# Optimization experiments

Measured on AMD Instinct MI355X. Metric: run time of the kernel, lower is better.

Reference implementation:

```python
import jax, jax.numpy as jnp
import numpy as np

HEADS = 2
C1 = 33    # per-head out channels, conv1
C2 = 550   # per-head out channels, conv2


def _lin_params(key, fan_in, fan_out):
    kw, kb = jax.random.split(key)
    scale = 1.0 / np.sqrt(fan_in)
    W = jax.random.uniform(kw, (fan_in, fan_out), jnp.float32, -scale, scale)
    b = jax.random.uniform(kb, (fan_out,), jnp.float32, -scale, scale)
    return W, b


def transformer_conv(x, src, dst, Wq, bq, Wk, bk, Wv, bv, Ws, bs, heads, out_ch):
    """PyG TransformerConv (concat=True, root_weight=True, beta=False)."""
    N = x.shape[0]
    q = (x @ Wq + bq).reshape(N, heads, out_ch)  # query of target node i
    k = (x @ Wk + bk).reshape(N, heads, out_ch)  # key of source node j
    v = (x @ Wv + bv).reshape(N, heads, out_ch)  # value of source node j
    # attention logits per edge: [E, H]
    alpha = jnp.einsum('ehc,ehc->eh', q[dst], k[src]) / jnp.sqrt(jnp.float32(out_ch))
    # segment softmax over incoming edges of each dst node
    m = jax.lax.stop_gradient(jax.ops.segment_max(alpha, dst, num_segments=N))  # [N,H]
    e = jnp.exp(alpha - m[dst])
    denom = jax.ops.segment_sum(e, dst, num_segments=N)  # [N,H]
    a = e / denom[dst]
    # weighted scatter-aggregate of source values: [N,H,C]
    out = jax.ops.segment_sum(a[..., None] * v[src], dst, num_segments=N)
    out = out.reshape(N, heads * out_ch)
    # root/skip connection
    out = out + x @ Ws + bs
    return out


def setup_inputs() -> dict:
    key = jax.random.key(0)
    ks = jax.random.split(key, 10)
    N, E, IN = 20000, 120000, 256
    x = jax.random.normal(ks[0], (N, IN), jnp.float32)
    edge_index = jax.random.randint(ks[1], (2, E), 0, N, jnp.int64 if jax.config.jax_enable_x64 else jnp.int32)
    d = {'x': x, 'edge_index': edge_index}
    # conv1: IN -> heads*C1
    d['Wq1'], d['bq1'] = _lin_params(ks[2], IN, HEADS * C1)
    d['Wk1'], d['bk1'] = _lin_params(ks[3], IN, HEADS * C1)
    d['Wv1'], d['bv1'] = _lin_params(ks[4], IN, HEADS * C1)
    d['Ws1'], d['bs1'] = _lin_params(ks[5], IN, HEADS * C1)
    # conv2: heads*C1 -> heads*C2
    IN2 = HEADS * C1
    d['Wq2'], d['bq2'] = _lin_params(ks[6], IN2, HEADS * C2)
    d['Wk2'], d['bk2'] = _lin_params(ks[7], IN2, HEADS * C2)
    d['Wv2'], d['bv2'] = _lin_params(ks[8], IN2, HEADS * C2)
    d['Ws2'], d['bs2'] = _lin_params(ks[9], IN2, HEADS * C2)
    return d


def reference(x, edge_index, Wq1, bq1, Wk1, bk1, Wv1, bv1, Ws1, bs1,
              Wq2, bq2, Wk2, bk2, Wv2, bv2, Ws2, bs2):
    src, dst = edge_index[0], edge_index[1]
    h = transformer_conv(x, src, dst, Wq1, bq1, Wk1, bk1, Wv1, bv1, Ws1, bs1, HEADS, C1)
    h = transformer_conv(h, src, dst, Wq2, bq2, Wk2, bk2, Wv2, bv2, Ws2, bs2, HEADS, C2)
    # x.view(N, 550, heads).max(dim=2) -- faithful to the original reshape layout
    h = h.reshape(h.shape[0], C2, HEADS)
    return jnp.max(h, axis=2)
```

## Files before the change

kernel.cpp:

```cpp
#include <hip/hip_runtime.h>
#include <math.h>

#define HEADS 2
#define C1    33
#define C2    550
#define D1    66
#define D2    1100
#define IN1   256
#define PROJW 288
#define KU    224
#define N2P   1152
#define KZ    96
#define ZW    144

typedef __attribute__((ext_vector_type(8))) short bfrag;
typedef __attribute__((ext_vector_type(4))) float f32x4;

__device__ inline unsigned short f2bf(float f) {
    unsigned int u = __float_as_uint(f);
    u += 0x7FFFu + ((u >> 16) & 1u);
    return (unsigned short)(u >> 16);
}

__device__ inline int xcd_slot(int bid, int slots) {
    return (bid >> 3) + (bid & 7) * slots;
}

__global__ void k_cvt(const float* __restrict__ x, unsigned short* __restrict__ xb, int total4) {
    int i = blockIdx.x * blockDim.x + threadIdx.x;
    if (i >= total4) return;
    float4 v = ((const float4*)x)[i];
    ushort4 o;
    o.x = f2bf(v.x); o.y = f2bf(v.y); o.z = f2bf(v.z); o.w = f2bf(v.w);
    ((ushort4*)xb)[i] = o;
}

__global__ void k_prep1(const float* __restrict__ Wq, const float* __restrict__ bq,
                        const float* __restrict__ Wk, const float* __restrict__ bk,
                        const float* __restrict__ Wv, const float* __restrict__ bv,
                        const float* __restrict__ Ws, const float* __restrict__ bs,
                        unsigned short* __restrict__ Wt1, float* __restrict__ bcat) {
    int c = blockIdx.x;
    int k = threadIdx.x;
    float val = 0.f, bia = 0.f;
    if (c < 4 * D1) {
        int m = c / D1, j = c % D1;
        const float* W; const float* B;
        switch (m) {
            case 0: W = Wq; B = bq; break;
            case 1: W = Wk; B = bk; break;
            case 2: W = Wv; B = bv; break;
            default: W = Ws; B = bs; break;
        }
        val = W[(size_t)k * D1 + j];
        bia = B[j];
    }
    Wt1[(size_t)c * IN1 + k] = f2bf(val);
    if (k == 0) bcat[c] = bia;
}

__global__ void k_prep2(const float* __restrict__ Wv2, const float* __restrict__ bv2,
                        const float* __restrict__ Ws2, const float* __restrict__ bs2,
                        unsigned short* __restrict__ W2t,
                        float* __restrict__ bvp, float* __restrict__ bsp) {
    int c = blockIdx.x;
    int k = threadIdx.x;
    if (k < KU) {
        float val = 0.f;
        if (c < D2) {
            int h = (c >= C2) ? 1 : 0;
            if (!h) {
                if (k < 66) val = Wv2[(size_t)k * D2 + c];
                else if (k >= 132 && k < 198) val = Ws2[(size_t)(k - 132) * D2 + c];
            } else {
                if (k >= 66 && k < 132) val = Wv2[(size_t)(k - 66) * D2 + c];
                else if (k >= 132 && k < 198) val = Ws2[(size_t)(k - 132) * D2 + c];
            }
        }
        W2t[(size_t)c * KU + k] = f2bf(val);
    }
    if (k == 0) {
        bvp[c] = (c < D2) ? bv2[c] : 0.f;
        bsp[c] = (c < D2) ? bs2[c] : 0.f;
    }
}

__global__ void k_hist(const int* __restrict__ dst, int E, int* __restrict__ cnt) {
    int e = blockIdx.x * blockDim.x + threadIdx.x;
    if (e < E) atomicAdd(&cnt[dst[e]], 1);
}

__global__ void k_scan(const int* __restrict__ cnt, int* __restrict__ roff,
                       int* __restrict__ pos, int N) {
    __shared__ int wsum[16];
    __shared__ int carry_s;
    int tid = threadIdx.x, wid = tid >> 6, lane = tid & 63;
    if (tid == 0) { carry_s = 0; roff[0] = 0; }
    __syncthreads();
    for (int base = 0; base < N; base += 1024) {
        int i = base + tid;
        int v = (i < N) ? cnt[i] : 0;
        int x = v;
        #pragma unroll
        for (int s = 1; s < 64; s <<= 1) {
            int t = __shfl_up(x, s, 64);
            if (lane >= s) x += t;
        }
        if (lane == 63) wsum[wid] = x;
        __syncthreads();
        if (tid < 16) {
            int y = wsum[tid];
            #pragma unroll
            for (int s = 1; s < 16; s <<= 1) {
                int t = __shfl_up(y, s, 16);
                if (tid >= s) y += t;
            }
            wsum[tid] = y;
        }
        __syncthreads();
        int carry = carry_s;
        int incl = carry + (wid ? wsum[wid - 1] : 0) + x;
        if (i < N) { roff[i + 1] = incl; pos[i] = incl - v; }
        __syncthreads();
        if (tid == 0) carry_s = carry + wsum[15];
        __syncthreads();
    }
}

__global__ void k_fill(const int* __restrict__ src, const int* __restrict__ dst, int E,
                       int* __restrict__ pos, int* __restrict__ elist) {
    int e = blockIdx.x * blockDim.x + threadIdx.x;
    if (e < E) {
        int slot = atomicAdd(&pos[dst[e]], 1);
        elist[slot] = src[e];
    }
}

__global__ __launch_bounds__(256, 2) void k_mm1(
        const unsigned short* __restrict__ A, const unsigned short* __restrict__ B,
        const float* __restrict__ bias, float* __restrict__ proj, int N,
        int nRow, int slots) {
    __shared__ __align__(16) short bs[8 * 4 * 96 * 8];
    int s = xcd_slot(blockIdx.x, slots);
    if (s >= nRow * 3) return;
    int rowt = s / 3, g = s - rowt * 3;
    int cbase = g * 96;
    int tid = threadIdx.x;
    for (int i = tid; i < 3072; i += 256) {
        int ks = i / 384, r = i % 384;
        int lk = r / 96, col = r % 96;
        *(bfrag*)&bs[i * 8] = *(const bfrag*)(B + (size_t)(cbase + col) * IN1 + ks * 32 + lk * 8);
    }
    int wave = tid >> 6, lane = tid & 63;
    int lr = lane & 15, lk = lane >> 4;
    int rbase = rowt * 128 + wave * 32;
    int ar[2];
    #pragma unroll
    for (int mi = 0; mi < 2; mi++) {
        int r = rbase + mi * 16 + lr;
        ar[mi] = (r < N) ? r : (N - 1);
    }
    bfrag a[2][8];
    #pragma unroll
    for (int mi = 0; mi < 2; mi++)
        #pragma unroll
        for (int ks = 0; ks < 8; ks++)
            a[mi][ks] = *(const bfrag*)(A + (size_t)ar[mi] * IN1 + ks * 32 + lk * 8);
    __syncthreads();
    f32x4 acc[2][6];
    #pragma unroll
    for (int mi = 0; mi < 2; mi++)
        #pragma unroll
        for (int ni = 0; ni < 6; ni++) acc[mi][ni] = (f32x4){0.f, 0.f, 0.f, 0.f};
    #pragma unroll
    for (int ks = 0; ks < 8; ks++) {
        bfrag b[6];
        #pragma unroll
        for (int ni = 0; ni < 6; ni++)
            b[ni] = *(const bfrag*)&bs[ks * 3072 + lk * 768 + (ni * 16 + lr) * 8];
        #pragma unroll
        for (int mi = 0; mi < 2; mi++)
            #pragma unroll
            for (int ni = 0; ni < 6; ni++)
                acc[mi][ni] = __builtin_amdgcn_mfma_f32_16x16x32_bf16(a[mi][ks], b[ni], acc[mi][ni], 0, 0, 0);
    }
    #pragma unroll
    for (int mi = 0; mi < 2; mi++) {
        #pragma unroll
        for (int ni = 0; ni < 6; ni++) {
            int col = cbase + ni * 16 + lr;
            float bia = bias[col];
            #pragma unroll
            for (int r = 0; r < 4; r++) {
                int row = rbase + mi * 16 + lk * 4 + r;
                if (row < N) proj[(size_t)row * PROJW + col] = acc[mi][ni][r] + bia;
            }
        }
    }
}

__global__ __launch_bounds__(128) void k_conv1(
        const float* __restrict__ proj, const int* __restrict__ roff,
        const int* __restrict__ elist, float* __restrict__ h1,
        unsigned short* __restrict__ h1b, int N) {
    int n = blockIdx.x;
    int h = threadIdx.x >> 6;
    int lane = threadIdx.x & 63;
    size_t pb = (size_t)n * PROJW;
    bool ok = (lane < C1);
    float my_q = ok ? proj[pb + h * C1 + lane] : 0.f;
    float s1v  = ok ? proj[pb + 198 + h * C1 + lane] : 0.f;
    float m = -INFINITY, lsum = 0.f, acc = 0.f;
    int e0 = roff[n], e1 = roff[n + 1];
    const float isc = 0.17407765595569785f;
    int e = e0;
    for (; e + 1 < e1; e += 2) {
        int sa = elist[e], sb = elist[e + 1];
        size_t ba = (size_t)sa * PROJW, bb = (size_t)sb * PROJW;
        float ka = ok ? proj[ba + 66 + h * C1 + lane] : 0.f;
        float va = ok ? proj[ba + 132 + h * C1 + lane] : 0.f;
        float kb = ok ? proj[bb + 66 + h * C1 + lane] : 0.f;
        float vb = ok ? proj[bb + 132 + h * C1 + lane] : 0.f;
        float pa = my_q * ka, pbv = my_q * kb;
        #pragma unroll
        for (int off = 32; off >= 1; off >>= 1) {
            pa  += __shfl_xor(pa, off, 64);
            pbv += __shfl_xor(pbv, off, 64);
        }
        float aa = pa * isc, ab = pbv * isc;
        float mp = fmaxf(aa, ab);
        float ea = __expf(aa - mp), eb = __expf(ab - mp);
        float lp = ea + eb, ap = ea * va + eb * vb;
        float mnew = fmaxf(m, mp);
        float sc = __expf(m - mnew), sp = __expf(mp - mnew);
        lsum = lsum * sc + lp * sp;
        acc  = acc * sc + ap * sp;
        m = mnew;
    }
    if (e < e1) {
        int s = elist[e];
        size_t sb = (size_t)s * PROJW;
        float kv = ok ? proj[sb + 66 + h * C1 + lane] : 0.f;
        float vv = ok ? proj[sb + 132 + h * C1 + lane] : 0.f;
        float prod = my_q * kv;
        #pragma unroll
        for (int off = 32; off >= 1; off >>= 1) prod += __shfl_xor(prod, off, 64);
        float alpha = prod * isc;
        float mnew = fmaxf(m, alpha);
        float sc = __expf(m - mnew);
        float p = __expf(alpha - mnew);
        lsum = lsum * sc + p;
        acc  = acc * sc + p * vv;
        m = mnew;
    }
    if (ok) {
        float res = (lsum > 0.f) ? acc / lsum : 0.f;
        float val = res + s1v;
        h1[(size_t)n * D1 + h * C1 + lane] = val;
        h1b[(size_t)n * KZ + h * C1 + lane] = f2bf(val);
    } else if (h == 1 && lane >= C1 && lane < C1 + 30) {
        h1b[(size_t)n * KZ + D1 + (lane - C1)] = 0;
    }
}

__global__ __launch_bounds__(256) void k_precomp(
        const float* __restrict__ Wq2, const float* __restrict__ bq2,
        const float* __restrict__ Wk2, const float* __restrict__ bk2,
        float* __restrict__ G, float* __restrict__ wqbk,
        float* __restrict__ wkbq, float* __restrict__ cc) {
    int wave = threadIdx.x >> 6, lane = threadIdx.x & 63;
    int j = blockIdx.x * 4 + wave;
    if (j >= 8978) return;
    const float *u, *v;
    float* outp;
    if (j < 8976) {
        int h = j / 4488;
        int r = j % 4488;
        int a = r / 68, b = r % 68;
        if (b < 66)      { u = Wq2 + (size_t)a * D2 + h * C2; v = Wk2 + (size_t)b * D2 + h * C2; outp = &G[h * 4356 + a * 66 + b]; }
        else if (b == 66){ u = Wq2 + (size_t)a * D2 + h * C2; v = bk2 + h * C2;                  outp = &wqbk[h * 66 + a]; }
        else             { u = Wk2 + (size_t)a * D2 + h * C2; v = bq2 + h * C2;                  outp = &wkbq[h * 66 + a]; }
    } else {
        int h = j - 8976;
        u = bq2 + h * C2; v = bk2 + h * C2; outp = &cc[h];
    }
    float acc = 0.f;
    for (int c = lane; c < C2; c += 64) acc += u[c] * v[c];
    #pragma unroll
    for (int off = 32; off >= 1; off >>= 1) acc += __shfl_xor(acc, off, 64);
    if (lane == 0) *outp = acc;
}

__global__ void k_prepz(const float* __restrict__ G, const float* __restrict__ wqbk,
                        const float* __restrict__ wkbq, unsigned short* __restrict__ GBt) {
    int r = blockIdx.x;
    int k = threadIdx.x;
    float v = 0.f;
    if (k < D1) {
        if (r < 132) v = G[r * D1 + k];
        else if (r < 134) v = wqbk[(r - 132) * D1 + k];
        else if (r < 136) v = wkbq[(r - 134) * D1 + k];
    }
    GBt[r * KZ + k] = f2bf(v);
}

__global__ __launch_bounds__(256) void k_mmz(
        const unsigned short* __restrict__ A, const unsigned short* __restrict__ B,
        float* __restrict__ Z, int N, int nRow, int slots) {
    int s = xcd_slot(blockIdx.x, slots);
    if (s >= nRow * 2) return;
    int rowt = s >> 1, g = s & 1;
    int wave = threadIdx.x >> 6, lane = threadIdx.x & 63;
    int lr = lane & 15, lk = lane >> 4;
    int rbase = rowt * 64 + (wave >> 1) * 32;
    int cbase = g * 96 + (wave & 1) * 48;
    f32x4 acc[2][3];
    #pragma unroll
    for (int i = 0; i < 2; i++)
        #pragma unroll
        for (int j = 0; j < 3; j++) acc[i][j] = (f32x4){0.f, 0.f, 0.f, 0.f};
    int ar[2];
    #pragma unroll
    for (int mi = 0; mi < 2; mi++) {
        int r = rbase + mi * 16 + lr;
        ar[mi] = (r < N) ? r : (N - 1);
    }
    #pragma unroll
    for (int ks = 0; ks < 3; ks++) {
        bfrag a[2], b[3];
        #pragma unroll
        for (int mi = 0; mi < 2; mi++)
            a[mi] = *(const bfrag*)(A + (size_t)ar[mi] * KZ + ks * 32 + lk * 8);
        #pragma unroll
        for (int ni = 0; ni < 3; ni++)
            b[ni] = *(const bfrag*)(B + (size_t)(cbase + ni * 16 + lr) * KZ + ks * 32 + lk * 8);
        #pragma unroll
        for (int mi = 0; mi < 2; mi++)
            #pragma unroll
            for (int ni = 0; ni < 3; ni++)
                acc[mi][ni] = __builtin_amdgcn_mfma_f32_16x16x32_bf16(a[mi], b[ni], acc[mi][ni], 0, 0, 0);
    }
    #pragma unroll
    for (int mi = 0; mi < 2; mi++) {
        #pragma unroll
        for (int ni = 0; ni < 3; ni++) {
            int col = cbase + ni * 16 + lr;
            if (col >= 136) continue;
            #pragma unroll
            for (int r = 0; r < 4; r++) {
                int row = rbase + mi * 16 + lk * 4 + r;
                if (row < N) Z[(size_t)row * ZW + col] = acc[mi][ni][r];
            }
        }
    }
}

__global__ __launch_bounds__(128) void k_conv2(
        const float* __restrict__ h1, const float* __restrict__ Z,
        const float* __restrict__ cc, const int* __restrict__ roff,
        const int* __restrict__ elist, unsigned short* __restrict__ U,
        float* __restrict__ flag, int N) {
    int n = blockIdx.x;
    int h = threadIdx.x >> 6;
    int lane = threadIdx.x & 63;
    int c0 = lane, c1 = lane + 64;
    bool ok1 = (c1 < D1);
    float hd0 = h1[(size_t)n * D1 + c0];
    float hd1 = ok1 ? h1[(size_t)n * D1 + c1] : 0.f;
    float adv = Z[(size_t)n * ZW + 132 + h] + cc[h];
    float m = -INFINITY, lsum = 0.f, a0 = 0.f, a1 = 0.f;
    int e0 = roff[n], e1 = roff[n + 1];
    const float isc = 0.04264014327112209f;
    int e = e0;
    for (; e + 1 < e1; e += 2) {
        int sa = elist[e], sb = elist[e + 1];
        const float* za = Z + (size_t)sa * ZW;
        const float* zb = Z + (size_t)sb * ZW;
        float pa = hd0 * za[h * D1 + c0] + (ok1 ? hd1 * za[h * D1 + c1] : 0.f);
        float pb = hd0 * zb[h * D1 + c0] + (ok1 ? hd1 * zb[h * D1 + c1] : 0.f);
        #pragma unroll
        for (int off = 32; off >= 1; off >>= 1) {
            pa += __shfl_xor(pa, off, 64);
            pb += __shfl_xor(pb, off, 64);
        }
        float aa = (pa + adv + za[134 + h]) * isc;
        float ab = (pb + adv + zb[134 + h]) * isc;
        float va0 = h1[(size_t)sa * D1 + c0];
        float va1 = ok1 ? h1[(size_t)sa * D1 + c1] : 0.f;
        float vb0 = h1[(size_t)sb * D1 + c0];
        float vb1 = ok1 ? h1[(size_t)sb * D1 + c1] : 0.f;
        float mp = fmaxf(aa, ab);
        float ea = __expf(aa - mp), eb = __expf(ab - mp);
        float lp = ea + eb;
        float ap0 = ea * va0 + eb * vb0;
        float ap1 = ea * va1 + eb * vb1;
        float mnew = fmaxf(m, mp);
        float sc = __expf(m - mnew), sp = __expf(mp - mnew);
        lsum = lsum * sc + lp * sp;
        a0 = a0 * sc + ap0 * sp;
        a1 = a1 * sc + ap1 * sp;
        m = mnew;
    }
    if (e < e1) {
        int s = elist[e];
        const float* zr = Z + (size_t)s * ZW;
        float prod = hd0 * zr[h * D1 + c0] + (ok1 ? hd1 * zr[h * D1 + c1] : 0.f);
        #pragma unroll
        for (int off = 32; off >= 1; off >>= 1) prod += __shfl_xor(prod, off, 64);
        float alpha = (prod + adv + zr[134 + h]) * isc;
        float mnew = fmaxf(m, alpha);
        float sc = __expf(m - mnew);
        float p = __expf(alpha - mnew);
        lsum = lsum * sc + p;
        float v0 = h1[(size_t)s * D1 + c0];
        float vv1 = ok1 ? h1[(size_t)s * D1 + c1] : 0.f;
        a0 = a0 * sc + p * v0;
        a1 = a1 * sc + p * vv1;
        m = mnew;
    }
    float inv = (lsum > 0.f) ? 1.f / lsum : 0.f;
    size_t ub = (size_t)n * KU;
    U[ub + h * D1 + c0] = f2bf(a0 * inv);
    if (ok1) U[ub + h * D1 + c1] = f2bf(a1 * inv);
    if (h == 0) {
        U[ub + 132 + c0] = f2bf(hd0);
        if (ok1) U[ub + 132 + c1] = f2bf(hd1);
    } else if (lane < KU - 198) {
        U[ub + 198 + lane] = 0;
    }
    if (lane == 0) flag[n * 2 + h] = (lsum > 0.f) ? 1.f : 0.f;
}

__global__ __launch_bounds__(256, 2) void k_mm2(
        const unsigned short* __restrict__ A, const unsigned short* __restrict__ B,
        const float* __restrict__ bvp, const float* __restrict__ bsp,
        const float* __restrict__ flag, float* __restrict__ out, int N,
        int nRow, int slots) {
    __shared__ __align__(16) short bs[7 * 4 * 96 * 8];
    int s = xcd_slot(blockIdx.x, slots);
    if (s >= nRow * 12) return;
    int rowt = s / 12, g = s - rowt * 12;
    int cbase = g * 96;
    int tid = threadIdx.x;
    for (int i = tid; i < 2688; i += 256) {
        int ks = i / 384, r = i % 384;
        int lk = r / 96, col = r % 96;
        *(bfrag*)&bs[i * 8] = *(const bfrag*)(B + (size_t)(cbase + col) * KU + ks * 32 + lk * 8);
    }
    int wave = tid >> 6, lane = tid & 63;
    int lr = lane & 15, lk = lane >> 4;
    int rbase = rowt * 128 + wave * 32;
    int ar[2];
    #pragma unroll
    for (int mi = 0; mi < 2; mi++) {
        int r = rbase + mi * 16 + lr;
        ar[mi] = (r < N) ? r : (N - 1);
    }
    bfrag a[2][7];
    #pragma unroll
    for (int mi = 0; mi < 2; mi++)
        #pragma unroll
        for (int ks = 0; ks < 7; ks++)
            a[mi][ks] = *(const bfrag*)(A + (size_t)ar[mi] * KU + ks * 32 + lk * 8);
    __syncthreads();
    f32x4 acc[2][6];
    #pragma unroll
    for (int mi = 0; mi < 2; mi++)
        #pragma unroll
        for (int ni = 0; ni < 6; ni++) acc[mi][ni] = (f32x4){0.f, 0.f, 0.f, 0.f};
    #pragma unroll
    for (int ks = 0; ks < 7; ks++) {
        bfrag b[6];
        #pragma unroll
        for (int ni = 0; ni < 6; ni++)
            b[ni] = *(const bfrag*)&bs[ks * 3072 + lk * 768 + (ni * 16 + lr) * 8];
        #pragma unroll
        for (int mi = 0; mi < 2; mi++)
            #pragma unroll
            for (int ni = 0; ni < 6; ni++)
                acc[mi][ni] = __builtin_amdgcn_mfma_f32_16x16x32_bf16(a[mi][ks], b[ni], acc[mi][ni], 0, 0, 0);
    }
    #pragma unroll
    for (int mi = 0; mi < 2; mi++) {
        #pragma unroll
        for (int ni = 0; ni < 6; ni++) {
            int col = cbase + ni * 16 + lr;
            float bv = bvp[col], bs_ = bsp[col];
            int hh = (col >= C2) ? 1 : 0;
            #pragma unroll
            for (int r = 0; r < 4; r++) {
                int row = rbase + mi * 16 + lk * 4 + r;
                int fr = (row < N) ? row : 0;
                float val = acc[mi][ni][r] + flag[fr * 2 + hh] * bv + bs_;
                float oth = __shfl_xor(val, 1, 64);
                if (row < N && col < D2 && !(col & 1))
                    out[(size_t)row * C2 + (col >> 1)] = fmaxf(val, oth);
            }
        }
    }
}

extern "C" void kernel_launch(void* const* d_in, const int* in_sizes, int n_in,
                              void* d_out, int out_size, void* d_ws, size_t ws_size,
                              hipStream_t stream) {
    const float* x  = (const float*)d_in[0];
    const int*   ei = (const int*)d_in[1];
    int N = in_sizes[0] / IN1;
    int E = in_sizes[1] / 2;
    const int* src = ei;
    const int* dst = ei + E;

    const float *Wq1 = (const float*)d_in[2],  *bq1 = (const float*)d_in[3];
    const float *Wk1 = (const float*)d_in[4],  *bk1 = (const float*)d_in[5];
    const float *Wv1 = (const float*)d_in[6],  *bv1 = (const float*)d_in[7];
    const float *Ws1 = (const float*)d_in[8],  *bs1 = (const float*)d_in[9];
    const float *Wq2 = (const float*)d_in[10], *bq2 = (const float*)d_in[11];
    const float *Wk2 = (const float*)d_in[12], *bk2 = (const float*)d_in[13];
    const float *Wv2 = (const float*)d_in[14], *bv2 = (const float*)d_in[15];
    const float *Ws2 = (const float*)d_in[16], *bs2 = (const float*)d_in[17];

    char* w = (char*)d_ws;
    size_t off = 0;
    auto take = [&](size_t bytes) { size_t o = off; off = (off + bytes + 255) & ~(size_t)255; return o; };

    unsigned short* xb = (unsigned short*)(w + take((size_t)N * IN1 * 2));
    size_t proj_off = take((size_t)N * PROJW * 4);
    float* proj = (float*)(w + proj_off);
    float* Z = proj;
    unsigned short* U = (unsigned short*)(w + proj_off + (size_t)N * ZW * 4);
    float* h1   = (float*)(w + take((size_t)N * D1 * 4));
    unsigned short* h1b = (unsigned short*)(w + take((size_t)N * KZ * 2));
    float* flag = (float*)(w + take((size_t)N * 2 * 4));
    float* G    = (float*)(w + take((size_t)2 * D1 * D1 * 4));
    float* wqbk = (float*)(w + take(2 * D1 * 4));
    float* wkbq = (float*)(w + take(2 * D1 * 4));
    float* cc   = (float*)(w + take(2 * 4));
    unsigned short* GBt = (unsigned short*)(w + take((size_t)192 * KZ * 2));
    unsigned short* Wt1 = (unsigned short*)(w + take((size_t)PROJW * IN1 * 2));
    float* bcat = (float*)(w + take(PROJW * 4));
    unsigned short* W2t = (unsigned short*)(w + take((size_t)N2P * KU * 2));
    float* bvp  = (float*)(w + take(N2P * 4));
    float* bsp  = (float*)(w + take(N2P * 4));
    int* cnt   = (int*)(w + take((size_t)N * 4));
    int* roff  = (int*)(w + take((size_t)(N + 1) * 4));
    int* pos   = (int*)(w + take((size_t)N * 4));
    int* elist = (int*)(w + take((size_t)E * 4));

    hipMemsetAsync(cnt, 0, (size_t)N * sizeof(int), stream);
    k_hist<<<(E + 255) / 256, 256, 0, stream>>>(dst, E, cnt);
    k_scan<<<1, 1024, 0, stream>>>(cnt, roff, pos, N);
    k_fill<<<(E + 255) / 256, 256, 0, stream>>>(src, dst, E, pos, elist);

    k_cvt<<<(N * IN1 / 4 + 255) / 256, 256, 0, stream>>>(x, xb, N * IN1 / 4);
    k_prep1<<<PROJW, 256, 0, stream>>>(Wq1, bq1, Wk1, bk1, Wv1, bv1, Ws1, bs1, Wt1, bcat);
    k_prep2<<<N2P, 256, 0, stream>>>(Wv2, bv2, Ws2, bs2, W2t, bvp, bsp);
    k_precomp<<<(8978 + 3) / 4, 256, 0, stream>>>(Wq2, bq2, Wk2, bk2, G, wqbk, wkbq, cc);
    k_prepz<<<192, KZ, 0, stream>>>(G, wqbk, wkbq, GBt);

    int nRow1 = (N + 127) / 128;
    int tot1  = nRow1 * 3;
    int slots1 = (tot1 + 7) / 8;
    int nRowZ = (N + 63) / 64;
    int totZ  = nRowZ * 2;
    int slotsZ = (totZ + 7) / 8;
    int nRow2 = (N + 127) / 128;
    int tot2  = nRow2 * 12;
    int slots2 = (tot2 + 7) / 8;

    k_mm1<<<slots1 * 8, 256, 0, stream>>>(xb, Wt1, bcat, proj, N, nRow1, slots1);
    k_conv1<<<N, 128, 0, stream>>>(proj, roff, elist, h1, h1b, N);

    k_mmz<<<slotsZ * 8, 256, 0, stream>>>(h1b, GBt, Z, N, nRowZ, slotsZ);

    k_conv2<<<N, 128, 0, stream>>>(h1, Z, cc, roff, elist, U, flag, N);

    k_mm2<<<slots2 * 8, 256, 0, stream>>>(U, W2t, bvp, bsp, flag, (float*)d_out, N, nRow2, slots2);
}
```

Before: 196.3 us.

## Pre-swizzle weight matrices into MFMA fragment layout and drop LDS staging

The weight-prep kernels now write the bf16 weight matrices directly in the per-k-step, per-lane fragment order the MFMA loops consume. The GEMM kernels (mm1, mm2, mmz) read B fragments straight from global memory with coalesced 16-byte loads instead of staging them through shared memory behind a barrier, and the launch-bounds occupancy hint is relaxed. The edge-aggregation loops in conv1 and conv2 are also unrolled to process four edges per iteration with a merged online-softmax update, giving more memory-level parallelism. The cost is that repeated B fragment reads now depend on L1/L2 caching rather than LDS, and the unrolled loops use more registers.

```diff
diff --git a/kernel.cpp b/kernel.cpp
--- a/kernel.cpp
+++ b/kernel.cpp
@@ -40,9 +40,14 @@
                         const float* __restrict__ Wv, const float* __restrict__ bv,
                         const float* __restrict__ Ws, const float* __restrict__ bs,
                         unsigned short* __restrict__ Wt1, float* __restrict__ bcat) {
-    int c = blockIdx.x;
-    int k = threadIdx.x;
-    float val = 0.f, bia = 0.f;
+    int bid = blockIdx.x;
+    int lk = bid & 3, t = bid >> 2;
+    int ks = t & 7, g = t >> 3;
+    int col = threadIdx.x;
+    int c = g * 96 + col;
+    int k0 = ks * 32 + lk * 8;
+    short vals[8];
+    float bia = 0.f;
     if (c < 4 * D1) {
         int m = c / D1, j = c % D1;
         const float* W; const float* B;
@@ -52,24 +57,34 @@
             case 2: W = Wv; B = bv; break;
             default: W = Ws; B = bs; break;
         }
-        val = W[(size_t)k * D1 + j];
+        #pragma unroll
+        for (int e = 0; e < 8; e++) vals[e] = (short)f2bf(W[(size_t)(k0 + e) * D1 + j]);
         bia = B[j];
-    }
-    Wt1[(size_t)c * IN1 + k] = f2bf(val);
-    if (k == 0) bcat[c] = bia;
+    } else {
+        #pragma unroll
+        for (int e = 0; e < 8; e++) vals[e] = 0;
+    }
+    *(bfrag*)&Wt1[((size_t)bid * 96 + col) * 8] = *(bfrag*)vals;
+    if (ks == 0 && lk == 0) bcat[c] = bia;
 }
 
 __global__ void k_prep2(const float* __restrict__ Wv2, const float* __restrict__ bv2,
                         const float* __restrict__ Ws2, const float* __restrict__ bs2,
                         unsigned short* __restrict__ W2t,
                         float* __restrict__ bvp, float* __restrict__ bsp) {
-    int c = blockIdx.x;
-    int k = threadIdx.x;
-    if (k < KU) {
+    int bid = blockIdx.x;
+    int lk = bid & 3, t = bid >> 2;
+    int ks = t % 7, g = t / 7;
+    int col = threadIdx.x;
+    int c = g * 96 + col;
+    int k0 = ks * 32 + lk * 8;
+    short vals[8];
+    #pragma unroll
+    for (int e = 0; e < 8; e++) {
+        int k = k0 + e;
         float val = 0.f;
         if (c < D2) {
-            int h = (c >= C2) ? 1 : 0;
-            if (!h) {
+            if (c < C2) {
                 if (k < 66) val = Wv2[(size_t)k * D2 + c];
                 else if (k >= 132 && k < 198) val = Ws2[(size_t)(k - 132) * D2 + c];
             } else {
@@ -77,9 +92,10 @@
                 else if (k >= 132 && k < 198) val = Ws2[(size_t)(k - 132) * D2 + c];
             }
         }
-        W2t[(size_t)c * KU + k] = f2bf(val);
-    }
-    if (k == 0) {
+        vals[e] = (short)f2bf(val);
+    }
+    *(bfrag*)&W2t[((size_t)bid * 96 + col) * 8] = *(bfrag*)vals;
+    if (ks == 0 && lk == 0) {
         bvp[c] = (c < D2) ? bv2[c] : 0.f;
         bsp[c] = (c < D2) ? bs2[c] : 0.f;
     }
@@ -136,22 +152,15 @@
     }
 }
 
-__global__ __launch_bounds__(256, 2) void k_mm1(
+__global__ __launch_bounds__(256) void k_mm1(
         const unsigned short* __restrict__ A, const unsigned short* __restrict__ B,
         const float* __restrict__ bias, float* __restrict__ proj, int N,
         int nRow, int slots) {
-    __shared__ __align__(16) short bs[8 * 4 * 96 * 8];
     int s = xcd_slot(blockIdx.x, slots);
     if (s >= nRow * 3) return;
     int rowt = s / 3, g = s - rowt * 3;
     int cbase = g * 96;
-    int tid = threadIdx.x;
-    for (int i = tid; i < 3072; i += 256) {
-        int ks = i / 384, r = i % 384;
-        int lk = r / 96, col = r % 96;
-        *(bfrag*)&bs[i * 8] = *(const bfrag*)(B + (size_t)(cbase + col) * IN1 + ks * 32 + lk * 8);
-    }
-    int wave = tid >> 6, lane = tid & 63;
+    int wave = threadIdx.x >> 6, lane = threadIdx.x & 63;
     int lr = lane & 15, lk = lane >> 4;
     int rbase = rowt * 128 + wave * 32;
     int ar[2];
@@ -166,7 +175,6 @@
         #pragma unroll
         for (int ks = 0; ks < 8; ks++)
             a[mi][ks] = *(const bfrag*)(A + (size_t)ar[mi] * IN1 + ks * 32 + lk * 8);
-    __syncthreads();
     f32x4 acc[2][6];
     #pragma unroll
     for (int mi = 0; mi < 2; mi++)
@@ -177,7 +185,7 @@
         bfrag b[6];
         #pragma unroll
         for (int ni = 0; ni < 6; ni++)
-            b[ni] = *(const bfrag*)&bs[ks * 3072 + lk * 768 + (ni * 16 + lr) * 8];
+            b[ni] = *(const bfrag*)(B + (size_t)(g * 8 + ks) * 3072 + lk * 768 + (ni * 16 + lr) * 8);
         #pragma unroll
         for (int mi = 0; mi < 2; mi++)
             #pragma unroll
@@ -207,20 +215,53 @@
     int h = threadIdx.x >> 6;
     int lane = threadIdx.x & 63;
     size_t pb = (size_t)n * PROJW;
+    int hc = h * C1;
     bool ok = (lane < C1);
-    float my_q = ok ? proj[pb + h * C1 + lane] : 0.f;
-    float s1v  = ok ? proj[pb + 198 + h * C1 + lane] : 0.f;
+    float my_q = ok ? proj[pb + hc + lane] : 0.f;
+    float s1v  = ok ? proj[pb + 198 + hc + lane] : 0.f;
     float m = -INFINITY, lsum = 0.f, acc = 0.f;
     int e0 = roff[n], e1 = roff[n + 1];
     const float isc = 0.17407765595569785f;
     int e = e0;
+    for (; e + 3 < e1; e += 4) {
+        int s0 = elist[e], s1 = elist[e + 1], s2 = elist[e + 2], s3 = elist[e + 3];
+        size_t b0 = (size_t)s0 * PROJW, b1 = (size_t)s1 * PROJW;
+        size_t b2 = (size_t)s2 * PROJW, b3 = (size_t)s3 * PROJW;
+        float k0 = ok ? proj[b0 + 66 + hc + lane] : 0.f;
+        float k1 = ok ? proj[b1 + 66 + hc + lane] : 0.f;
+        float k2 = ok ? proj[b2 + 66 + hc + lane] : 0.f;
+        float k3 = ok ? proj[b3 + 66 + hc + lane] : 0.f;
+        float v0 = ok ? proj[b0 + 132 + hc + lane] : 0.f;
+        float v1 = ok ? proj[b1 + 132 + hc + lane] : 0.f;
+        float v2 = ok ? proj[b2 + 132 + hc + lane] : 0.f;
+        float v3 = ok ? proj[b3 + 132 + hc + lane] : 0.f;
+        float p0 = my_q * k0, p1 = my_q * k1, p2 = my_q * k2, p3 = my_q * k3;
+        #pragma unroll
+        for (int off = 32; off >= 1; off >>= 1) {
+            p0 += __shfl_xor(p0, off, 64);
+            p1 += __shfl_xor(p1, off, 64);
+            p2 += __shfl_xor(p2, off, 64);
+            p3 += __shfl_xor(p3, off, 64);
+        }
+        float a0 = p0 * isc, a1 = p1 * isc, a2 = p2 * isc, a3 = p3 * isc;
+        float mp = fmaxf(fmaxf(a0, a1), fmaxf(a2, a3));
+        float e0v = __expf(a0 - mp), e1v = __expf(a1 - mp);
+        float e2v = __expf(a2 - mp), e3v = __expf(a3 - mp);
+        float lp = (e0v + e1v) + (e2v + e3v);
+        float ap = (e0v * v0 + e1v * v1) + (e2v * v2 + e3v * v3);
+        float mnew = fmaxf(m, mp);
+        float sc = __expf(m - mnew), sp = __expf(mp - mnew);
+        lsum = lsum * sc + lp * sp;
+        acc  = acc * sc + ap * sp;
+        m = mnew;
+    }
     for (; e + 1 < e1; e += 2) {
         int sa = elist[e], sb = elist[e + 1];
         size_t ba = (size_t)sa * PROJW, bb = (size_t)sb * PROJW;
-        float ka = ok ? proj[ba + 66 + h * C1 + lane] : 0.f;
-        float va = ok ? proj[ba + 132 + h * C1 + lane] : 0.f;
-        float kb = ok ? proj[bb + 66 + h * C1 + lane] : 0.f;
-        float vb = ok ? proj[bb + 132 + h * C1 + lane] : 0.f;
+        float ka = ok ? proj[ba + 66 + hc + lane] : 0.f;
+        float va = ok ? proj[ba + 132 + hc + lane] : 0.f;
+        float kb = ok ? proj[bb + 66 + hc + lane] : 0.f;
+        float vb = ok ? proj[bb + 132 + hc + lane] : 0.f;
         float pa = my_q * ka, pbv = my_q * kb;
         #pragma unroll
         for (int off = 32; off >= 1; off >>= 1) {
@@ -240,8 +281,8 @@
     if (e < e1) {
         int s = elist[e];
         size_t sb = (size_t)s * PROJW;
-        float kv = ok ? proj[sb + 66 + h * C1 + lane] : 0.f;
-        float vv = ok ? proj[sb + 132 + h * C1 + lane] : 0.f;
+        float kv = ok ? proj[sb + 66 + hc + lane] : 0.f;
+        float vv = ok ? proj[sb + 132 + hc + lane] : 0.f;
         float prod = my_q * kv;
         #pragma unroll
         for (int off = 32; off >= 1; off >>= 1) prod += __shfl_xor(prod, off, 64);
@@ -256,8 +297,8 @@
     if (ok) {
         float res = (lsum > 0.f) ? acc / lsum : 0.f;
         float val = res + s1v;
-        h1[(size_t)n * D1 + h * C1 + lane] = val;
-        h1b[(size_t)n * KZ + h * C1 + lane] = f2bf(val);
+        h1[(size_t)n * D1 + hc + lane] = val;
+        h1b[(size_t)n * KZ + hc + lane] = f2bf(val);
     } else if (h == 1 && lane >= C1 && lane < C1 + 30) {
         h1b[(size_t)n * KZ + D1 + (lane - C1)] = 0;
     }
@@ -293,15 +334,25 @@
 
 __global__ void k_prepz(const float* __restrict__ G, const float* __restrict__ wqbk,
                         const float* __restrict__ wkbq, unsigned short* __restrict__ GBt) {
-    int r = blockIdx.x;
-    int k = threadIdx.x;
-    float v = 0.f;
-    if (k < D1) {
-        if (r < 132) v = G[r * D1 + k];
-        else if (r < 134) v = wqbk[(r - 132) * D1 + k];
-        else if (r < 136) v = wkbq[(r - 134) * D1 + k];
-    }
-    GBt[r * KZ + k] = f2bf(v);
+    int bid = blockIdx.x;
+    int lk = bid & 3, t = bid >> 2;
+    int ks = t % 3, g = t / 3;
+    int col = threadIdx.x;
+    int r = g * 96 + col;
+    int k0 = ks * 32 + lk * 8;
+    short vals[8];
+    #pragma unroll
+    for (int e = 0; e < 8; e++) {
+        int k = k0 + e;
+        float v = 0.f;
+        if (k < D1) {
+            if (r < 132) v = G[r * D1 + k];
+            else if (r < 134) v = wqbk[(r - 132) * D1 + k];
+            else if (r < 136) v = wkbq[(r - 134) * D1 + k];
+        }
+        vals[e] = (short)f2bf(v);
+    }
+    *(bfrag*)&GBt[((size_t)bid * 96 + col) * 8] = *(bfrag*)vals;
 }
 
 __global__ __launch_bounds__(256) void k_mmz(
@@ -313,7 +364,8 @@
     int wave = threadIdx.x >> 6, lane = threadIdx.x & 63;
     int lr = lane & 15, lk = lane >> 4;
     int rbase = rowt * 64 + (wave >> 1) * 32;
-    int cbase = g * 96 + (wave & 1) * 48;
+    int ch = (wave & 1) * 48;
+    int cbase = g * 96 + ch;
     f32x4 acc[2][3];
     #pragma unroll
     for (int i = 0; i < 2; i++)
@@ -333,7 +385,7 @@
             a[mi] = *(const bfrag*)(A + (size_t)ar[mi] * KZ + ks * 32 + lk * 8);
         #pragma unroll
         for (int ni = 0; ni < 3; ni++)
-            b[ni] = *(const bfrag*)(B + (size_t)(cbase + ni * 16 + lr) * KZ + ks * 32 + lk * 8);
+            b[ni] = *(const bfrag*)(B + (size_t)(g * 3 + ks) * 3072 + lk * 768 + (ch + ni * 16 + lr) * 8);
         #pragma unroll
         for (int mi = 0; mi < 2; mi++)
             #pragma unroll
@@ -371,13 +423,56 @@
     float m = -INFINITY, lsum = 0.f, a0 = 0.f, a1 = 0.f;
     int e0 = roff[n], e1 = roff[n + 1];
     const float isc = 0.04264014327112209f;
+    int hD = h * D1;
     int e = e0;
+    for (; e + 3 < e1; e += 4) {
+        int s0 = elist[e], s1 = elist[e + 1], s2 = elist[e + 2], s3 = elist[e + 3];
+        const float* z0 = Z + (size_t)s0 * ZW;
+        const float* z1 = Z + (size_t)s1 * ZW;
+        const float* z2 = Z + (size_t)s2 * ZW;
+        const float* z3 = Z + (size_t)s3 * ZW;
+        float p0 = hd0 * z0[hD + c0] + (ok1 ? hd1 * z0[hD + c1] : 0.f);
+        float p1 = hd0 * z1[hD + c0] + (ok1 ? hd1 * z1[hD + c1] : 0.f);
+        float p2 = hd0 * z2[hD + c0] + (ok1 ? hd1 * z2[hD + c1] : 0.f);
+        float p3 = hd0 * z3[hD + c0] + (ok1 ? hd1 * z3[hD + c1] : 0.f);
+        #pragma unroll
+        for (int off = 32; off >= 1; off >>= 1) {
+            p0 += __shfl_xor(p0, off, 64);
+            p1 += __shfl_xor(p1, off, 64);
+            p2 += __shfl_xor(p2, off, 64);
+            p3 += __shfl_xor(p3, off, 64);
+        }
+        float al0 = (p0 + adv + z0[134 + h]) * isc;
+        float al1 = (p1 + adv + z1[134 + h]) * isc;
+        float al2 = (p2 + adv + z2[134 + h]) * isc;
+        float al3 = (p3 + adv + z3[134 + h]) * isc;
+        float va00 = h1[(size_t)s0 * D1 + c0];
+        float va01 = ok1 ? h1[(size_t)s0 * D1 + c1] : 0.f;
+        float va10 = h1[(size_t)s1 * D1 + c0];
+        float va11 = ok1 ? h1[(size_t)s1 * D1 + c1] : 0.f;
+        float va20 = h1[(size_t)s2 * D1 + c0];
+        float va21 = ok1 ? h1[(size_t)s2 * D1 + c1] : 0.f;
+        float va30 = h1[(size_t)s3 * D1 + c0];
+        float va31 = ok1 ? h1[(size_t)s3 * D1 + c1] : 0.f;
+        float mp = fmaxf(fmaxf(al0, al1), fmaxf(al2, al3));
+        float e0v = __expf(al0 - mp), e1v = __expf(al1 - mp);
+        float e2v = __expf(al2 - mp), e3v = __expf(al3 - mp);
+        float lp = (e0v + e1v) + (e2v + e3v);
+        float ap0 = (e0v * va00 + e1v * va10) + (e2v * va20 + e3v * va30);
+        float ap1 = (e0v * va01 + e1v * va11) + (e2v * va21 + e3v * va31);
+        float mnew = fmaxf(m, mp);
+        float sc = __expf(m - mnew), sp = __expf(mp - mnew);
+        lsum = lsum * sc + lp * sp;
+        a0 = a0 * sc + ap0 * sp;
+        a1 = a1 * sc + ap1 * sp;
+        m = mnew;
+    }
     for (; e + 1 < e1; e += 2) {
         int sa = elist[e], sb = elist[e + 1];
         const float* za = Z + (size_t)sa * ZW;
         const float* zb = Z + (size_t)sb * ZW;
-        float pa = hd0 * za[h * D1 + c0] + (ok1 ? hd1 * za[h * D1 + c1] : 0.f);
-        float pb = hd0 * zb[h * D1 + c0] + (ok1 ? hd1 * zb[h * D1 + c1] : 0.f);
+        float pa = hd0 * za[hD + c0] + (ok1 ? hd1 * za[hD + c1] : 0.f);
+        float pb = hd0 * zb[hD + c0] + (ok1 ? hd1 * zb[hD + c1] : 0.f);
         #pragma unroll
         for (int off = 32; off >= 1; off >>= 1) {
             pa += __shfl_xor(pa, off, 64);
@@ -404,7 +499,7 @@
     if (e < e1) {
         int s = elist[e];
         const float* zr = Z + (size_t)s * ZW;
-        float prod = hd0 * zr[h * D1 + c0] + (ok1 ? hd1 * zr[h * D1 + c1] : 0.f);
+        float prod = hd0 * zr[hD + c0] + (ok1 ? hd1 * zr[hD + c1] : 0.f);
         #pragma unroll
         for (int off = 32; off >= 1; off >>= 1) prod += __shfl_xor(prod, off, 64);
         float alpha = (prod + adv + zr[134 + h]) * isc;
@@ -420,8 +515,8 @@
     }
     float inv = (lsum > 0.f) ? 1.f / lsum : 0.f;
     size_t ub = (size_t)n * KU;
-    U[ub + h * D1 + c0] = f2bf(a0 * inv);
-    if (ok1) U[ub + h * D1 + c1] = f2bf(a1 * inv);
+    U[ub + hD + c0] = f2bf(a0 * inv);
+    if (ok1) U[ub + hD + c1] = f2bf(a1 * inv);
     if (h == 0) {
         U[ub + 132 + c0] = f2bf(hd0);
         if (ok1) U[ub + 132 + c1] = f2bf(hd1);
@@ -431,23 +526,16 @@
     if (lane == 0) flag[n * 2 + h] = (lsum > 0.f) ? 1.f : 0.f;
 }
 
-__global__ __launch_bounds__(256, 2) void k_mm2(
+__global__ __launch_bounds__(256) void k_mm2(
         const unsigned short* __restrict__ A, const unsigned short* __restrict__ B,
         const float* __restrict__ bvp, const float* __restrict__ bsp,
         const float* __restrict__ flag, float* __restrict__ out, int N,
         int nRow, int slots) {
-    __shared__ __align__(16) short bs[7 * 4 * 96 * 8];
     int s = xcd_slot(blockIdx.x, slots);
     if (s >= nRow * 12) return;
     int rowt = s / 12, g = s - rowt * 12;
     int cbase = g * 96;
-    int tid = threadIdx.x;
-    for (int i = tid; i < 2688; i += 256) {
-        int ks = i / 384, r = i % 384;
-        int lk = r / 96, col = r % 96;
-        *(bfrag*)&bs[i * 8] = *(const bfrag*)(B + (size_t)(cbase + col) * KU + ks * 32 + lk * 8);
-    }
-    int wave = tid >> 6, lane = tid & 63;
+    int wave = threadIdx.x >> 6, lane = threadIdx.x & 63;
     int lr = lane & 15, lk = lane >> 4;
     int rbase = rowt * 128 + wave * 32;
     int ar[2];
@@ -462,7 +550,6 @@
         #pragma unroll
         for (int ks = 0; ks < 7; ks++)
             a[mi][ks] = *(const bfrag*)(A + (size_t)ar[mi] * KU + ks * 32 + lk * 8);
-    __syncthreads();
     f32x4 acc[2][6];
     #pragma unroll
     for (int mi = 0; mi < 2; mi++)
@@ -473,7 +560,7 @@
         bfrag b[6];
         #pragma unroll
         for (int ni = 0; ni < 6; ni++)
-            b[ni] = *(const bfrag*)&bs[ks * 3072 + lk * 768 + (ni * 16 + lr) * 8];
+            b[ni] = *(const bfrag*)(B + (size_t)(g * 7 + ks) * 3072 + lk * 768 + (ni * 16 + lr) * 8);
         #pragma unroll
         for (int mi = 0; mi < 2; mi++)
             #pragma unroll
@@ -535,10 +622,10 @@
     float* wqbk = (float*)(w + take(2 * D1 * 4));
     float* wkbq = (float*)(w + take(2 * D1 * 4));
     float* cc   = (float*)(w + take(2 * 4));
-    unsigned short* GBt = (unsigned short*)(w + take((size_t)192 * KZ * 2));
-    unsigned short* Wt1 = (unsigned short*)(w + take((size_t)PROJW * IN1 * 2));
+    unsigned short* GBt = (unsigned short*)(w + take((size_t)24 * 96 * 8 * 2));
+    unsigned short* Wt1 = (unsigned short*)(w + take((size_t)96 * 96 * 8 * 2));
     float* bcat = (float*)(w + take(PROJW * 4));
-    unsigned short* W2t = (unsigned short*)(w + take((size_t)N2P * KU * 2));
+    unsigned short* W2t = (unsigned short*)(w + take((size_t)336 * 96 * 8 * 2));
     float* bvp  = (float*)(w + take(N2P * 4));
     float* bsp  = (float*)(w + take(N2P * 4));
     int* cnt   = (int*)(w + take((size_t)N * 4));
@@ -552,10 +639,10 @@
     k_fill<<<(E + 255) / 256, 256, 0, stream>>>(src, dst, E, pos, elist);
 
     k_cvt<<<(N * IN1 / 4 + 255) / 256, 256, 0, stream>>>(x, xb, N * IN1 / 4);
-    k_prep1<<<PROJW, 256, 0, stream>>>(Wq1, bq1, Wk1, bk1, Wv1, bv1, Ws1, bs1, Wt1, bcat);
-    k_prep2<<<N2P, 256, 0, stream>>>(Wv2, bv2, Ws2, bs2, W2t, bvp, bsp);
+    k_prep1<<<96, 96, 0, stream>>>(Wq1, bq1, Wk1, bk1, Wv1, bv1, Ws1, bs1, Wt1, bcat);
+    k_prep2<<<336, 96, 0, stream>>>(Wv2, bv2, Ws2, bs2, W2t, bvp, bsp);
     k_precomp<<<(8978 + 3) / 4, 256, 0, stream>>>(Wq2, bq2, Wk2, bk2, G, wqbk, wkbq, cc);
-    k_prepz<<<192, KZ, 0, stream>>>(G, wqbk, wkbq, GBt);
+    k_prepz<<<24, 96, 0, stream>>>(G, wqbk, wkbq, GBt);
 
     int nRow1 = (N + 127) / 128;
     int tot1  = nRow1 * 3;
```

Result: no change. 192.5 us (-1.9%).
